# Kernel tuning notes

Hardware: AMD Instinct MI355X
Metric: run time of the kernel (lower is better)

## Reference

```python
import jax, jax.numpy as jnp
import numpy as np


def setup_inputs() -> dict:
    key = jax.random.key(0)
    ks = jax.random.split(key, 6)
    N, C, T, V = 32, 64, 128, 25
    F = C * T * V  # 204800
    H = 256
    E = 4
    stdv0 = 1.0 / np.sqrt(F)
    stdv1 = 1.0 / np.sqrt(H)
    stdvA = 1.0 / np.sqrt(V)
    return {
        "x": jax.random.normal(ks[0], (N, C, T, V), dtype=jnp.float32),
        "W0": jax.random.uniform(ks[1], (F, H), jnp.float32, -stdv0, stdv0),
        "b0": jnp.zeros((H,), jnp.float32),
        "W1": jax.random.uniform(ks[2], (H, H), jnp.float32, -stdv1, stdv1),
        "b1": jnp.zeros((H,), jnp.float32),
        "W2": jax.random.uniform(ks[3], (H, E), jnp.float32, -stdv1, stdv1),
        "b2": jnp.zeros((E,), jnp.float32),
        "A": jax.random.uniform(ks[4], (E, T, V, V), jnp.float32, -stdvA, stdvA),
    }


def reference(x, W0, b0, W1, b1, W2, b2, A):
    N = x.shape[0]
    # Gating MLP (dropout treated as identity / eval mode)
    g = x.reshape(N, -1)                      # [N, C*T*V]
    h = jax.nn.elu(g @ W0 + b0)               # [N, 256]
    h = jax.nn.elu(h @ W1 + b1)               # [N, 256]
    logits = h @ W2 + b2                      # [N, 4]
    w = jax.nn.softmax(logits, axis=1)        # [N, 4]
    # Mixture of adjacency experts: AS[n,t,v,w] = sum_e w[n,e] * A[e,t,v,w]
    AS = jnp.einsum('ne,etvw->ntvw', w, A)    # [N, T, V, V]
    # Batched graph convolution
    out = jnp.einsum('nctv,ntvw->nctw', x, AS)
    return out
```

## Files before the change

### kernel.cpp

```cpp
#include <hip/hip_runtime.h>
#include <math.h>

#define Nn 32
#define Cc 64
#define Tt 128
#define Vv 25
#define Kk 204800
#define Hh 256
#define Ee 4
#define KC 400
#define NBLK_A 512

__device__ __forceinline__ float elu1(float v) { return v > 0.0f ? v : expm1f(v); }

__global__ __launch_bounds__(256) void kA(const float* __restrict__ x,
                                          const float* __restrict__ W0,
                                          float* __restrict__ partials) {
  __shared__ float xs[Nn][KC];
  const int tid = threadIdx.x;
  const int b = blockIdx.x;
  const int k0 = b * KC;

  for (int j = tid; j < Nn * (KC / 4); j += 256) {
    int n = j / (KC / 4);
    int col = j - n * (KC / 4);
    float4 v = *(const float4*)(x + (size_t)n * Kk + k0 + col * 4);
    *(float4*)&xs[n][col * 4] = v;
  }
  __syncthreads();

  const int hq = tid & 63;
  const int p  = tid >> 6;
  const int n0 = p * 8;
  const float* W0p = W0 + (size_t)k0 * Hh + hq * 4;

  float acc[8][4];
  #pragma unroll
  for (int i = 0; i < 8; ++i)
    #pragma unroll
    for (int c = 0; c < 4; ++c) acc[i][c] = 0.0f;

  for (int kk = 0; kk < KC; kk += 4) {
    float xv[8][4];
    #pragma unroll
    for (int i = 0; i < 8; ++i)
      *(float4*)xv[i] = *(const float4*)&xs[n0 + i][kk];
    #pragma unroll
    for (int u = 0; u < 4; ++u) {
      float4 w4 = *(const float4*)(W0p + (size_t)(kk + u) * Hh);
      #pragma unroll
      for (int i = 0; i < 8; ++i) {
        acc[i][0] = fmaf(xv[i][u], w4.x, acc[i][0]);
        acc[i][1] = fmaf(xv[i][u], w4.y, acc[i][1]);
        acc[i][2] = fmaf(xv[i][u], w4.z, acc[i][2]);
        acc[i][3] = fmaf(xv[i][u], w4.w, acc[i][3]);
      }
    }
  }
  #pragma unroll
  for (int i = 0; i < 8; ++i) {
    float4 o = make_float4(acc[i][0], acc[i][1], acc[i][2], acc[i][3]);
    *(float4*)&partials[((size_t)(b * Nn + n0 + i) << 8) + hq * 4] = o;
  }
}

__global__ __launch_bounds__(256) void kB1(const float* __restrict__ partials,
                                           const float* __restrict__ b0,
                                           float* __restrict__ hb) {
  const int n  = blockIdx.x >> 3;
  const int hc = blockIdx.x & 7;
  const int tid = threadIdx.x;
  const int hl = tid & 31;
  const int bsub = tid >> 5;
  const int h = hc * 32 + hl;
  float s = 0.0f;
  for (int j = 0; j < 64; ++j) {
    int b = bsub * 64 + j;
    s += partials[((size_t)(b * Nn + n) << 8) + h];
  }
  __shared__ float red[8][32];
  red[bsub][hl] = s;
  __syncthreads();
  if (tid < 32) {
    float tot = 0.0f;
    #pragma unroll
    for (int sI = 0; sI < 8; ++sI) tot += red[sI][tid];
    int hh = hc * 32 + tid;
    hb[n * Hh + hh] = elu1(tot + b0[hh]);
  }
}

__global__ __launch_bounds__(256) void kB2(const float* __restrict__ hb,
                                           const float* __restrict__ W1,
                                           const float* __restrict__ b1,
                                           const float* __restrict__ W2,
                                           const float* __restrict__ b2,
                                           float* __restrict__ wgt) {
  const int n = blockIdx.x;
  const int tid = threadIdx.x;
  __shared__ float hbs[Hh];
  hbs[tid] = hb[n * Hh + tid];
  __syncthreads();
  float s = b1[tid];
  for (int j = 0; j < Hh; ++j) s = fmaf(hbs[j], W1[j * Hh + tid], s);
  float h2 = elu1(s);
  float le[Ee];
  #pragma unroll
  for (int e = 0; e < Ee; ++e) le[e] = h2 * W2[tid * Ee + e];
  __shared__ float red[Ee][4];
  const int lane = tid & 63;
  const int wid  = tid >> 6;
  #pragma unroll
  for (int e = 0; e < Ee; ++e) {
    float v = le[e];
    for (int off = 32; off > 0; off >>= 1) v += __shfl_down(v, off, 64);
    if (lane == 0) red[e][wid] = v;
  }
  __syncthreads();
  if (tid == 0) {
    float lg[Ee];
    float m = -1e30f;
    #pragma unroll
    for (int e = 0; e < Ee; ++e) {
      lg[e] = red[e][0] + red[e][1] + red[e][2] + red[e][3] + b2[e];
      m = fmaxf(m, lg[e]);
    }
    float den = 0.0f;
    #pragma unroll
    for (int e = 0; e < Ee; ++e) { lg[e] = expf(lg[e] - m); den += lg[e]; }
    float inv = 1.0f / den;
    #pragma unroll
    for (int e = 0; e < Ee; ++e) wgt[n * Ee + e] = lg[e] * inv;
  }
}

__global__ __launch_bounds__(256) void kC(const float* __restrict__ x,
                                          const float* __restrict__ A,
                                          const float* __restrict__ wgt,
                                          float* __restrict__ out) {
  const int b = blockIdx.x;
  const int n = b >> 7;
  const int t = b & 127;
  __shared__ float AS[Vv * Vv];
  __shared__ float xsl[Cc * Vv];
  float wv[Ee];
  #pragma unroll
  for (int e = 0; e < Ee; ++e) wv[e] = wgt[n * Ee + e];

  for (int idx = threadIdx.x; idx < Vv * Vv; idx += 256) {
    float s = 0.0f;
    #pragma unroll
    for (int e = 0; e < Ee; ++e)
      s = fmaf(wv[e], A[(size_t)(e * Tt + t) * (Vv * Vv) + idx], s);
    AS[idx] = s;
  }
  const float* xb = x + (size_t)n * (Cc * Tt * Vv) + (size_t)t * Vv;
  for (int idx = threadIdx.x; idx < Cc * Vv; idx += 256) {
    int c = idx / Vv;
    int v = idx - c * Vv;
    xsl[idx] = xb[(size_t)c * (Tt * Vv) + v];
  }
  __syncthreads();
  float* ob = out + (size_t)n * (Cc * Tt * Vv) + (size_t)t * Vv;
  for (int idx = threadIdx.x; idx < Cc * Vv; idx += 256) {
    int c = idx / Vv;
    int w = idx - c * Vv;
    float s = 0.0f;
    #pragma unroll
    for (int v = 0; v < Vv; ++v)
      s = fmaf(xsl[c * Vv + v], AS[v * Vv + w], s);
    ob[(size_t)c * (Tt * Vv) + w] = s;
  }
}

extern "C" void kernel_launch(void* const* d_in, const int* in_sizes, int n_in,
                              void* d_out, int out_size, void* d_ws, size_t ws_size,
                              hipStream_t stream) {
  const float* x  = (const float*)d_in[0];
  const float* W0 = (const float*)d_in[1];
  const float* b0 = (const float*)d_in[2];
  const float* W1 = (const float*)d_in[3];
  const float* b1 = (const float*)d_in[4];
  const float* W2 = (const float*)d_in[5];
  const float* b2 = (const float*)d_in[6];
  const float* A  = (const float*)d_in[7];
  float* out = (float*)d_out;

  float* partials = (float*)d_ws;
  float* hb  = partials + (size_t)NBLK_A * Nn * Hh;
  float* wgt = hb + Nn * Hh;

  kA <<<NBLK_A, 256, 0, stream>>>(x, W0, partials);
  kB1<<<256,    256, 0, stream>>>(partials, b0, hb);
  kB2<<<Nn,     256, 0, stream>>>(hb, W1, b1, W2, b2, wgt);
  kC <<<Nn * Tt,256, 0, stream>>>(x, A, wgt, out);
}
```

Baseline: 386.6 us.

## Retile W0 GEMM and register-block the graph convolution kernel

The first GEMM kernel now splits K into 800 chunks of 256 instead of 512 chunks of 400, and each thread computes a 4x8 tile (4 samples by 8 hidden units) instead of 8x4. The partial-sum reduction is widened to match. The graph-convolution kernel handles two time steps per block. It stores x transposed and AS padded in shared memory and gives each thread a 4x4 register tile fed by float4 LDS reads, replacing the scalar dot products. This aims for more parallelism in the W0 stream and fewer shared-memory loads per FMA, at the cost of more partials traffic and some idle threads (wq==7).

```diff
diff --git a/kernel.cpp b/kernel.cpp
--- a/kernel.cpp
+++ b/kernel.cpp
@@ -8,8 +8,8 @@
 #define Kk 204800
 #define Hh 256
 #define Ee 4
-#define KC 400
-#define NBLK_A 512
+#define KC 256
+#define NBLK_A 800
 
 __device__ __forceinline__ float elu1(float v) { return v > 0.0f ? v : expm1f(v); }
 
@@ -21,46 +21,56 @@
   const int b = blockIdx.x;
   const int k0 = b * KC;
 
+  #pragma unroll
   for (int j = tid; j < Nn * (KC / 4); j += 256) {
-    int n = j / (KC / 4);
-    int col = j - n * (KC / 4);
-    float4 v = *(const float4*)(x + (size_t)n * Kk + k0 + col * 4);
-    *(float4*)&xs[n][col * 4] = v;
-  }
-  __syncthreads();
-
-  const int hq = tid & 63;
-  const int p  = tid >> 6;
-  const int n0 = p * 8;
-  const float* W0p = W0 + (size_t)k0 * Hh + hq * 4;
-
-  float acc[8][4];
-  #pragma unroll
-  for (int i = 0; i < 8; ++i)
-    #pragma unroll
-    for (int c = 0; c < 4; ++c) acc[i][c] = 0.0f;
+    int n = j >> 6;
+    int c4 = j & 63;
+    float4 v = *(const float4*)(x + (size_t)n * Kk + k0 + c4 * 4);
+    *(float4*)&xs[n][c4 * 4] = v;
+  }
+  __syncthreads();
+
+  const int hg = tid & 31;
+  const int np = tid >> 5;
+  const int h0 = hg * 8;
+  const int n0 = np * 4;
+  const float* W0p = W0 + (size_t)k0 * Hh + h0;
+
+  float acc[4][8];
+  #pragma unroll
+  for (int i = 0; i < 4; ++i)
+    #pragma unroll
+    for (int c = 0; c < 8; ++c) acc[i][c] = 0.0f;
 
   for (int kk = 0; kk < KC; kk += 4) {
-    float xv[8][4];
-    #pragma unroll
-    for (int i = 0; i < 8; ++i)
-      *(float4*)xv[i] = *(const float4*)&xs[n0 + i][kk];
+    float4 xv[4];
+    #pragma unroll
+    for (int i = 0; i < 4; ++i)
+      xv[i] = *(const float4*)&xs[n0 + i][kk];
     #pragma unroll
     for (int u = 0; u < 4; ++u) {
-      float4 w4 = *(const float4*)(W0p + (size_t)(kk + u) * Hh);
-      #pragma unroll
-      for (int i = 0; i < 8; ++i) {
-        acc[i][0] = fmaf(xv[i][u], w4.x, acc[i][0]);
-        acc[i][1] = fmaf(xv[i][u], w4.y, acc[i][1]);
-        acc[i][2] = fmaf(xv[i][u], w4.z, acc[i][2]);
-        acc[i][3] = fmaf(xv[i][u], w4.w, acc[i][3]);
+      const float* wp = W0p + (size_t)(kk + u) * Hh;
+      float4 wa = *(const float4*)(wp);
+      float4 wb = *(const float4*)(wp + 4);
+      #pragma unroll
+      for (int i = 0; i < 4; ++i) {
+        float xu = (u == 0) ? xv[i].x : (u == 1) ? xv[i].y : (u == 2) ? xv[i].z : xv[i].w;
+        acc[i][0] = fmaf(xu, wa.x, acc[i][0]);
+        acc[i][1] = fmaf(xu, wa.y, acc[i][1]);
+        acc[i][2] = fmaf(xu, wa.z, acc[i][2]);
+        acc[i][3] = fmaf(xu, wa.w, acc[i][3]);
+        acc[i][4] = fmaf(xu, wb.x, acc[i][4]);
+        acc[i][5] = fmaf(xu, wb.y, acc[i][5]);
+        acc[i][6] = fmaf(xu, wb.z, acc[i][6]);
+        acc[i][7] = fmaf(xu, wb.w, acc[i][7]);
       }
     }
   }
   #pragma unroll
-  for (int i = 0; i < 8; ++i) {
-    float4 o = make_float4(acc[i][0], acc[i][1], acc[i][2], acc[i][3]);
-    *(float4*)&partials[((size_t)(b * Nn + n0 + i) << 8) + hq * 4] = o;
+  for (int i = 0; i < 4; ++i) {
+    float* pp = partials + ((size_t)(b * Nn + n0 + i) << 8) + h0;
+    *(float4*)(pp)     = make_float4(acc[i][0], acc[i][1], acc[i][2], acc[i][3]);
+    *(float4*)(pp + 4) = make_float4(acc[i][4], acc[i][5], acc[i][6], acc[i][7]);
   }
 }
 
@@ -74,8 +84,8 @@
   const int bsub = tid >> 5;
   const int h = hc * 32 + hl;
   float s = 0.0f;
-  for (int j = 0; j < 64; ++j) {
-    int b = bsub * 64 + j;
+  for (int j = 0; j < 100; ++j) {
+    int b = bsub * 100 + j;
     s += partials[((size_t)(b * Nn + n) << 8) + h];
   }
   __shared__ float red[8][32];
@@ -134,42 +144,78 @@
   }
 }
 
+#define ASW 28
+#define XTS 68
 __global__ __launch_bounds__(256) void kC(const float* __restrict__ x,
                                           const float* __restrict__ A,
                                           const float* __restrict__ wgt,
                                           float* __restrict__ out) {
-  const int b = blockIdx.x;
-  const int n = b >> 7;
-  const int t = b & 127;
-  __shared__ float AS[Vv * Vv];
-  __shared__ float xsl[Cc * Vv];
+  const int blk = blockIdx.x;
+  const int n  = blk >> 6;
+  const int tp = blk & 63;
+  const int tid = threadIdx.x;
+  const int tsub = tid >> 7;
+  const int tl = tid & 127;
+  const int t = tp * 2 + tsub;
+
+  __shared__ float AS[2][Vv][ASW];
+  __shared__ float xT[2][Vv][XTS];
+
   float wv[Ee];
   #pragma unroll
   for (int e = 0; e < Ee; ++e) wv[e] = wgt[n * Ee + e];
 
-  for (int idx = threadIdx.x; idx < Vv * Vv; idx += 256) {
+  for (int idx = tl; idx < Vv * ASW; idx += 128) {
+    int v = idx / ASW;
+    int w = idx - v * ASW;
     float s = 0.0f;
-    #pragma unroll
-    for (int e = 0; e < Ee; ++e)
-      s = fmaf(wv[e], A[(size_t)(e * Tt + t) * (Vv * Vv) + idx], s);
-    AS[idx] = s;
+    if (w < Vv) {
+      #pragma unroll
+      for (int e = 0; e < Ee; ++e)
+        s = fmaf(wv[e], A[((size_t)(e * Tt + t) * Vv + v) * Vv + w], s);
+    }
+    AS[tsub][v][w] = s;
   }
   const float* xb = x + (size_t)n * (Cc * Tt * Vv) + (size_t)t * Vv;
-  for (int idx = threadIdx.x; idx < Cc * Vv; idx += 256) {
+  for (int idx = tl; idx < Cc * Vv; idx += 128) {
     int c = idx / Vv;
     int v = idx - c * Vv;
-    xsl[idx] = xb[(size_t)c * (Tt * Vv) + v];
-  }
-  __syncthreads();
-  float* ob = out + (size_t)n * (Cc * Tt * Vv) + (size_t)t * Vv;
-  for (int idx = threadIdx.x; idx < Cc * Vv; idx += 256) {
-    int c = idx / Vv;
-    int w = idx - c * Vv;
-    float s = 0.0f;
-    #pragma unroll
-    for (int v = 0; v < Vv; ++v)
-      s = fmaf(xsl[c * Vv + v], AS[v * Vv + w], s);
-    ob[(size_t)c * (Tt * Vv) + w] = s;
+    xT[tsub][v][c] = xb[(size_t)c * (Tt * Vv) + v];
+  }
+  __syncthreads();
+
+  const int ct = tl & 15;
+  const int wq = tl >> 4;
+  if (wq < 7) {
+    const int c0 = ct * 4;
+    const int w0 = wq * 4;
+    float acc[4][4];
+    #pragma unroll
+    for (int i = 0; i < 4; ++i)
+      #pragma unroll
+      for (int j = 0; j < 4; ++j) acc[i][j] = 0.0f;
+    #pragma unroll 5
+    for (int v = 0; v < Vv; ++v) {
+      float4 a4 = *(const float4*)&AS[tsub][v][w0];
+      float4 x4 = *(const float4*)&xT[tsub][v][c0];
+      const float xr[4] = {x4.x, x4.y, x4.z, x4.w};
+      const float ar[4] = {a4.x, a4.y, a4.z, a4.w};
+      #pragma unroll
+      for (int i = 0; i < 4; ++i)
+        #pragma unroll
+        for (int j = 0; j < 4; ++j)
+          acc[i][j] = fmaf(xr[i], ar[j], acc[i][j]);
+    }
+    #pragma unroll
+    for (int i = 0; i < 4; ++i) {
+      int c = c0 + i;
+      float* ob = out + ((size_t)(n * Cc + c) * Tt + t) * Vv;
+      #pragma unroll
+      for (int j = 0; j < 4; ++j) {
+        int w = w0 + j;
+        if (w < Vv) ob[w] = acc[i][j];
+      }
+    }
   }
 }
 
@@ -190,8 +236,8 @@
   float* hb  = partials + (size_t)NBLK_A * Nn * Hh;
   float* wgt = hb + Nn * Hh;
 
-  kA <<<NBLK_A, 256, 0, stream>>>(x, W0, partials);
-  kB1<<<256,    256, 0, stream>>>(partials, b0, hb);
-  kB2<<<Nn,     256, 0, stream>>>(hb, W1, b1, W2, b2, wgt);
-  kC <<<Nn * Tt,256, 0, stream>>>(x, A, wgt, out);
-}
+  kA <<<NBLK_A,  256, 0, stream>>>(x, W0, partials);
+  kB1<<<256,     256, 0, stream>>>(partials, b0, hb);
+  kB2<<<Nn,      256, 0, stream>>>(hb, W1, b1, W2, b2, wgt);
+  kC <<<Nn * 64, 256, 0, stream>>>(x, A, wgt, out);
+}
```

Result: slower. 426.7 us (+10.4%).
